# Optimization experiments

Hardware: AMD Instinct MI355X
Metric: run time of the kernel (lower is better)

Reference implementation:

```python
import jax, jax.numpy as jnp
import numpy as np

# ---- problem dims (match init_kwargs / input_specs) ----
B, N, ATOM = 128, 80, 16
HG, ENC_BLOCKS, ENC_HEADS, N_RBF = 512, 4, 8, 16
HID, DEC_LAYERS, DEC_HEADS = 256, 8, 8
KL_DIM, KL_WEIGHT = 6, 1e-6
NEG = -1e9


def layernorm(x, g, b, eps=1e-5):
    mu = x.mean(-1, keepdims=True)
    var = ((x - mu) ** 2).mean(-1, keepdims=True)
    return (x - mu) * jax.lax.rsqrt(var + eps) * g + b


def mha(x, qkv_w, qkv_b, out_w, out_b, bias, n_heads):
    # x: (B,S,D); bias: broadcastable to (B,H,S,S) additive attention bias/mask
    Bx, S, D = x.shape
    dh = D // n_heads
    q, k, v = jnp.split(x @ qkv_w + qkv_b, 3, axis=-1)
    q = q.reshape(Bx, S, n_heads, dh)
    k = k.reshape(Bx, S, n_heads, dh)
    v = v.reshape(Bx, S, n_heads, dh)
    logits = jnp.einsum('bqhd,bkhd->bhqk', q, k) * (1.0 / np.sqrt(dh)) + bias
    attn = jax.nn.softmax(logits, axis=-1)
    o = jnp.einsum('bhqk,bkhd->bqhd', attn, v).reshape(Bx, S, D)
    return o @ out_w + out_b


def sinusoid_posenc(seq_len, dim):
    pos = jnp.arange(seq_len, dtype=jnp.float32)[:, None]
    div = jnp.exp(jnp.arange(0, dim, 2, dtype=jnp.float32) * (-np.log(10000.0) / dim))
    ang = pos * div
    pe = jnp.zeros((seq_len, dim), jnp.float32)
    pe = pe.at[:, 0::2].set(jnp.sin(ang)).at[:, 1::2].set(jnp.cos(ang))
    return pe


def time_fourier(t, dim, max_len=200.0):
    half = dim // 2
    freqs = jnp.exp(jnp.arange(half, dtype=jnp.float32) * (-np.log(max_len) / half))
    ang = t[:, None] * max_len * freqs[None, :]
    return jnp.concatenate([jnp.sin(ang), jnp.cos(ang)], axis=-1)


def setup_inputs() -> dict:
    key = jax.random.key(0)
    ks = iter(jax.random.split(key, 64))
    nrm = lambda shp, s=0.02: jax.random.normal(next(ks), shp, jnp.float32) * s
    inp = {}
    inp['coord_ori'] = jax.random.normal(next(ks), (B, N, 3), jnp.float32)
    inp['atomics_ori'] = jax.nn.one_hot(jax.random.randint(next(ks), (B, N), 0, ATOM), ATOM, dtype=jnp.float32)
    lengths = jax.random.randint(next(ks), (B,), N // 2, N + 1)
    inp['padding_mask'] = jnp.arange(N)[None, :] >= lengths[:, None]
    inp['coord_t'] = jax.random.normal(next(ks), (B, N, 3), jnp.float32)
    inp['atomics_t'] = jax.nn.one_hot(jax.random.randint(next(ks), (B, N), 0, ATOM), ATOM, dtype=jnp.float32)
    inp['t'] = jax.random.uniform(next(ks), (B,), jnp.float32)
    # ---- GSRD encoder params (fully-connected graph attention blocks) ----
    inp['enc_embed_w'] = nrm((ATOM, HG))
    inp['rbf_w'] = nrm((ENC_BLOCKS, N_RBF, ENC_HEADS))
    inp['e_qkv_w'] = nrm((ENC_BLOCKS, HG, 3 * HG)); inp['e_qkv_b'] = jnp.zeros((ENC_BLOCKS, 3 * HG))
    inp['e_out_w'] = nrm((ENC_BLOCKS, HG, HG)); inp['e_out_b'] = jnp.zeros((ENC_BLOCKS, HG))
    inp['e_ff1_w'] = nrm((ENC_BLOCKS, HG, 4 * HG)); inp['e_ff1_b'] = jnp.zeros((ENC_BLOCKS, 4 * HG))
    inp['e_ff2_w'] = nrm((ENC_BLOCKS, 4 * HG, HG)); inp['e_ff2_b'] = jnp.zeros((ENC_BLOCKS, HG))
    inp['e_ln1_g'] = jnp.ones((ENC_BLOCKS, HG)); inp['e_ln1_b'] = jnp.zeros((ENC_BLOCKS, HG))
    inp['e_ln2_g'] = jnp.ones((ENC_BLOCKS, HG)); inp['e_ln2_b'] = jnp.zeros((ENC_BLOCKS, HG))
    # ---- projection / VAE bottleneck / decoder embeddings ----
    inp['enc_proj_w'] = nrm((HG, HID))
    inp['quant_w'] = nrm((HID, 2 * KL_DIM)); inp['quant_b'] = jnp.zeros((2 * KL_DIM,))
    inp['qout_w'] = nrm((KL_DIM, HID)); inp['qout_b'] = jnp.zeros((HID,))
    inp['cond_embed'] = nrm((2, HID))
    inp['lin_embed_w'] = nrm((3, HID))
    inp['atom_embed'] = nrm((ATOM, HID))
    # ---- decoder transformer (pre-norm, SiLU FFN) ----
    inp['d_qkv_w'] = nrm((DEC_LAYERS, HID, 3 * HID)); inp['d_qkv_b'] = jnp.zeros((DEC_LAYERS, 3 * HID))
    inp['d_out_w'] = nrm((DEC_LAYERS, HID, HID)); inp['d_out_b'] = jnp.zeros((DEC_LAYERS, HID))
    inp['d_ff1_w'] = nrm((DEC_LAYERS, HID, 4 * HID)); inp['d_ff1_b'] = jnp.zeros((DEC_LAYERS, 4 * HID))
    inp['d_ff2_w'] = nrm((DEC_LAYERS, 4 * HID, HID)); inp['d_ff2_b'] = jnp.zeros((DEC_LAYERS, HID))
    inp['d_ln1_g'] = jnp.ones((DEC_LAYERS, HID)); inp['d_ln1_b'] = jnp.zeros((DEC_LAYERS, HID))
    inp['d_ln2_g'] = jnp.ones((DEC_LAYERS, HID)); inp['d_ln2_b'] = jnp.zeros((DEC_LAYERS, HID))
    # ---- output heads ----
    inp['oc_ln_g'] = jnp.ones((HID,)); inp['oc_ln_b'] = jnp.zeros((HID,))
    inp['oc_w'] = nrm((HID, 3))
    inp['oa1_w'] = nrm((HID, HID)); inp['oa1_b'] = jnp.zeros((HID,))
    inp['oa2_w'] = nrm((HID, ATOM)); inp['oa2_b'] = jnp.zeros((ATOM,))
    return inp


def forward_impl(padding_mask, coord_ori, atomics_ori, coord_t, atomics_t, t,
                 enc_embed_w, rbf_w, e_qkv_w, e_qkv_b, e_out_w, e_out_b,
                 e_ff1_w, e_ff1_b, e_ff2_w, e_ff2_b, e_ln1_g, e_ln1_b, e_ln2_g, e_ln2_b,
                 enc_proj_w, quant_w, quant_b, qout_w, qout_b,
                 cond_embed, lin_embed_w, atom_embed,
                 d_qkv_w, d_qkv_b, d_out_w, d_out_b, d_ff1_w, d_ff1_b, d_ff2_w, d_ff2_b,
                 d_ln1_g, d_ln1_b, d_ln2_g, d_ln2_b,
                 oc_ln_g, oc_ln_b, oc_w, oa1_w, oa1_b, oa2_w, oa2_b):
    real = (~padding_mask).astype(jnp.float32)  # (B,N)
    # ===== encode_z: per-sample fully-connected graph GNN, expressed densely =====
    # The original builds (n*(n-1)) edges per molecule via meshgrid and runs an
    # edge-based encoder: equivalent to masked dense attention over (B,N,N) with
    # no self-loops and padded nodes removed.
    diff = coord_ori[:, :, None, :] - coord_ori[:, None, :, :]
    dist = jnp.sqrt((diff * diff).sum(-1) + 1e-12)                     # (B,N,N)
    centers = jnp.linspace(0.0, 10.0, N_RBF)
    rbf = jnp.exp(-2.0 * (dist[..., None] - centers) ** 2)             # (B,N,N,R)
    eye = jnp.eye(N, dtype=bool)
    emask = padding_mask[:, None, None, :] | eye[None, None, :, :]     # (B,1,N,N)
    mask_bias = jnp.where(emask, NEG, 0.0)
    h = atomics_ori @ enc_embed_w                                      # (B,N,HG)
    for i in range(ENC_BLOCKS):
        db = jnp.einsum('bqkr,rh->bhqk', rbf, rbf_w[i]) + mask_bias
        h = h + mha(layernorm(h, e_ln1_g[i], e_ln1_b[i]), e_qkv_w[i], e_qkv_b[i],
                    e_out_w[i], e_out_b[i], db, ENC_HEADS)
        f = layernorm(h, e_ln2_g[i], e_ln2_b[i])
        h = h + (jax.nn.silu(f @ e_ff1_w[i] + e_ff1_b[i]) @ e_ff2_w[i] + e_ff2_b[i])
    rep = h * real[..., None]                  # to_dense_batch zeros padded slots
    rep = rep @ enc_proj_w                     # (B,N,HID)
    # ---- VAE bottleneck (eval mode: z = mu) ----
    moments = rep @ quant_w + quant_b
    mu, logvar = jnp.split(moments, 2, axis=-1)
    z = mu
    kl_item = (1.0 + logvar - mu * mu - jnp.exp(logvar)) * real[..., None]
    kl_loss = -0.5 * jnp.mean(kl_item.sum(-1)) * KL_WEIGHT
    # ===== decode_z =====
    enc_emb = z @ qout_w + qout_b
    pe = sinusoid_posenc(N, HID)[None]         # (1,N,HID)
    enc_emb = (enc_emb + pe) * real[..., None]
    h_in = (coord_t @ lin_embed_w + atom_embed[atomics_t.argmax(-1)] + pe
            + time_fourier(t, HID)[:, None, :]) * real[..., None]
    x = jnp.concatenate([h_in, enc_emb], axis=1)                       # (B,2N,HID)
    x = x + jnp.concatenate([jnp.broadcast_to(cond_embed[0], (B, N, HID)),
                             jnp.broadcast_to(cond_embed[1], (B, N, HID))], axis=1)
    dmask = jnp.concatenate([padding_mask, padding_mask], axis=1)      # (B,2N)
    dbias = jnp.where(dmask, NEG, 0.0)[:, None, None, :]
    for i in range(DEC_LAYERS):
        x = x + mha(layernorm(x, d_ln1_g[i], d_ln1_b[i]), d_qkv_w[i], d_qkv_b[i],
                    d_out_w[i], d_out_b[i], dbias, DEC_HEADS)
        f = layernorm(x, d_ln2_g[i], d_ln2_b[i])
        x = x + (jax.nn.silu(f @ d_ff1_w[i] + d_ff1_b[i]) @ d_ff2_w[i] + d_ff2_b[i])
    h_out = x[:, :N, :] * real[..., None]
    coords = layernorm(h_out, oc_ln_g, oc_ln_b) @ oc_w
    atom_logits = jax.nn.silu(h_out @ oa1_w + oa1_b) @ oa2_w + oa2_b
    return coords, atom_logits, kl_loss


def reference(coord_ori, atomics_ori, padding_mask, coord_t, atomics_t, t,
              enc_embed_w, rbf_w, e_qkv_w, e_qkv_b, e_out_w, e_out_b,
              e_ff1_w, e_ff1_b, e_ff2_w, e_ff2_b, e_ln1_g, e_ln1_b, e_ln2_g, e_ln2_b,
              enc_proj_w, quant_w, quant_b, qout_w, qout_b,
              cond_embed, lin_embed_w, atom_embed,
              d_qkv_w, d_qkv_b, d_out_w, d_out_b, d_ff1_w, d_ff1_b, d_ff2_w, d_ff2_b,
              d_ln1_g, d_ln1_b, d_ln2_g, d_ln2_b,
              oc_ln_g, oc_ln_b, oc_w, oa1_w, oa1_b, oa2_w, oa2_b):
    return forward_impl(padding_mask, coord_ori, atomics_ori, coord_t, atomics_t, t,
                        enc_embed_w, rbf_w, e_qkv_w, e_qkv_b, e_out_w, e_out_b,
                        e_ff1_w, e_ff1_b, e_ff2_w, e_ff2_b, e_ln1_g, e_ln1_b, e_ln2_g, e_ln2_b,
                        enc_proj_w, quant_w, quant_b, qout_w, qout_b,
                        cond_embed, lin_embed_w, atom_embed,
                        d_qkv_w, d_qkv_b, d_out_w, d_out_b, d_ff1_w, d_ff1_b, d_ff2_w, d_ff2_b,
                        d_ln1_g, d_ln1_b, d_ln2_g, d_ln2_b,
                        oc_ln_g, oc_ln_b, oc_w, oa1_w, oa1_b, oa2_w, oa2_b)
```

## Files before the change

### kernel.cpp

```cpp
#include <hip/hip_runtime.h>
#include <hip/hip_bf16.h>
#include <math.h>

#define NBATCH 128
#define NATOM  80
#define SENC   80
#define SDEC   160
#define HGDIM  512
#define HIDDIM 256
#define NHEAD  8
#define ROWS_E (NBATCH*NATOM)
#define ROWS_D (NBATCH*SDEC)

typedef __hip_bfloat16 bf16;
typedef __attribute__((ext_vector_type(8))) short bf16x8;
typedef __attribute__((ext_vector_type(4))) float f32x4;

#define OFF_REAL 0ull
#define OFF_FLAG 10240ull
#define OFF_H    16384ull
#define OFF_QKVB (OFF_H   + 5242880ull)
#define OFF_DB   (OFF_QKVB+ 7864320ull)
#define OFF_LNB  (OFF_DB  + 6553600ull)
#define OFF_AOB  (OFF_LNB + 2621440ull)
#define OFF_MID  (OFF_AOB + 2621440ull)
#define OFF_MOM  (OFF_MID + 10485760ull)
#define OFF_KL   (OFF_MOM + 122880ull)
#define OFF_WT   (OFF_KL  + 64ull)
#define NEED_BYTES 184058112ull

#define WT_EQKV 0ull
#define WT_EOUT 3145728ull
#define WT_EFF1 4194304ull
#define WT_EFF2 8388608ull
#define WT_PROJ 12582912ull
#define WT_DQKV 12713984ull
#define WT_DOW  14286848ull
#define WT_DFF1 14811136ull
#define WT_DFF2 16908288ull
#define WT_OA1  19005440ull

static __device__ __forceinline__ float bu2f(unsigned int u){
  union{unsigned int i; float f;} x; x.i = u<<16; return x.f;
}
static __device__ __forceinline__ unsigned short f2bu(float f){
  union{bf16 h; unsigned short u;} x; x.h = __float2bfloat16(f); return x.u;
}

__global__ void k_maskmode(const unsigned char* __restrict__ m, int* __restrict__ flag){
  __shared__ int sh[256];
  int loc = 0;
  for(int i=threadIdx.x; i<ROWS_E; i+=256)
    if((i&3)!=0 && m[i]) loc = 1;
  sh[threadIdx.x] = loc;
  __syncthreads();
  if(threadIdx.x==0){
    int a=0;
    for(int j=0;j<256;j++) a |= sh[j];
    *flag = a;
  }
}

__global__ void k_real(const unsigned char* __restrict__ m, const int* __restrict__ flag,
                       float* __restrict__ real){
  int i = blockIdx.x*256 + threadIdx.x;
  if(i >= ROWS_E) return;
  int v = (*flag) ? (int)m[i] : ((const int*)m)[i];
  real[i] = v ? 0.f : 1.f;
}

__global__ void k_wsfail(float* __restrict__ out, float code){
  if(threadIdx.x==0) out[0] = code;
}

__global__ __launch_bounds__(256) void k_wt(const float* __restrict__ src,
    bf16* __restrict__ dst, int K, int N){
  __shared__ float t[32][33];
  const float* s = src + (size_t)blockIdx.z*K*N;
  bf16* d = dst + (size_t)blockIdx.z*K*N;
  int n0 = blockIdx.x*32, k0 = blockIdx.y*32;
  int tx = threadIdx.x & 31, ty = threadIdx.x >> 5;
  #pragma unroll
  for(int kk=0;kk<32;kk+=8)
    t[kk+ty][tx] = s[(size_t)(k0+kk+ty)*N + n0+tx];
  __syncthreads();
  #pragma unroll
  for(int nn=0;nn<32;nn+=8)
    d[(size_t)(n0+nn+ty)*K + k0+tx] = __float2bfloat16(t[tx][nn+ty]);
}

__global__ void k_embed(const float* __restrict__ atom, const float* __restrict__ W,
                        float* __restrict__ h){
  int idx = blockIdx.x*256 + threadIdx.x;
  if(idx >= ROWS_E*HGDIM) return;
  int row = idx >> 9, c = idx & 511;
  float s = 0.f;
  #pragma unroll
  for(int a=0;a<16;a++) s += atom[row*16+a] * W[a*HGDIM+c];
  h[idx] = s;
}

__global__ __launch_bounds__(256) void k_ln4(const float* __restrict__ x,
    const float* __restrict__ g, const float* __restrict__ bta,
    bf16* __restrict__ y, int D){
  int row = blockIdx.x*4 + (threadIdx.x>>6);
  int lane = threadIdx.x & 63;
  const float* xr = x + (size_t)row*D;
  int nch = D >> 8;
  float4 v[2];
  float s=0.f, s2=0.f;
  for(int j=0;j<nch;j++){
    v[j] = *(const float4*)&xr[j*256 + lane*4];
    s  += v[j].x+v[j].y+v[j].z+v[j].w;
    s2 += v[j].x*v[j].x+v[j].y*v[j].y+v[j].z*v[j].z+v[j].w*v[j].w;
  }
  #pragma unroll
  for(int o=32;o>0;o>>=1){ s += __shfl_xor(s,o); s2 += __shfl_xor(s2,o); }
  float mean = s / D;
  float var  = fmaxf(s2 / D - mean*mean, 0.f);
  float inv  = rsqrtf(var + 1e-5f);
  for(int j=0;j<nch;j++){
    int c = j*256 + lane*4;
    ushort4 o4;
    o4.x = f2bu((v[j].x-mean)*inv*g[c]   + bta[c]);
    o4.y = f2bu((v[j].y-mean)*inv*g[c+1] + bta[c+1]);
    o4.z = f2bu((v[j].z-mean)*inv*g[c+2] + bta[c+2]);
    o4.w = f2bu((v[j].w-mean)*inv*g[c+3] + bta[c+3]);
    *(ushort4*)&y[(size_t)row*D + c] = o4;
  }
}

__global__ __launch_bounds__(256) void k_ln4b(const bf16* __restrict__ x,
    const float* __restrict__ g, const float* __restrict__ bta,
    bf16* __restrict__ y, int D){
  int row = blockIdx.x*4 + (threadIdx.x>>6);
  int lane = threadIdx.x & 63;
  const unsigned short* xr = (const unsigned short*)(x + (size_t)row*D);
  int nch = D >> 8;
  float4 v[2];
  float s=0.f, s2=0.f;
  for(int j=0;j<nch;j++){
    ushort4 u = *(const ushort4*)&xr[j*256 + lane*4];
    v[j].x = bu2f(u.x); v[j].y = bu2f(u.y); v[j].z = bu2f(u.z); v[j].w = bu2f(u.w);
    s  += v[j].x+v[j].y+v[j].z+v[j].w;
    s2 += v[j].x*v[j].x+v[j].y*v[j].y+v[j].z*v[j].z+v[j].w*v[j].w;
  }
  #pragma unroll
  for(int o=32;o>0;o>>=1){ s += __shfl_xor(s,o); s2 += __shfl_xor(s2,o); }
  float mean = s / D;
  float var  = fmaxf(s2 / D - mean*mean, 0.f);
  float inv  = rsqrtf(var + 1e-5f);
  for(int j=0;j<nch;j++){
    int c = j*256 + lane*4;
    ushort4 o4;
    o4.x = f2bu((v[j].x-mean)*inv*g[c]   + bta[c]);
    o4.y = f2bu((v[j].y-mean)*inv*g[c+1] + bta[c+1]);
    o4.z = f2bu((v[j].z-mean)*inv*g[c+2] + bta[c+2]);
    o4.w = f2bu((v[j].w-mean)*inv*g[c+3] + bta[c+3]);
    *(ushort4*)&y[(size_t)row*D + c] = o4;
  }
}

__global__ void k_db(const float* __restrict__ coord, const float* __restrict__ real,
                     const float* __restrict__ rbfw, float* __restrict__ db){
  int idx = blockIdx.x*256 + threadIdx.x;
  if(idx >= NBATCH*SENC*SENC) return;
  int b = idx/(SENC*SENC), r = idx%(SENC*SENC), q = r/SENC, k = r%SENC;
  float out[NHEAD];
  bool masked = (real[b*NATOM+k]==0.f) || (k==q);
  if(masked){
    #pragma unroll
    for(int h=0;h<NHEAD;h++) out[h] = -1e9f;
  } else {
    float dx = coord[(b*NATOM+q)*3+0] - coord[(b*NATOM+k)*3+0];
    float dy = coord[(b*NATOM+q)*3+1] - coord[(b*NATOM+k)*3+1];
    float dz = coord[(b*NATOM+q)*3+2] - coord[(b*NATOM+k)*3+2];
    float d  = sqrtf(dx*dx+dy*dy+dz*dz + 1e-12f);
    #pragma unroll
    for(int h=0;h<NHEAD;h++) out[h]=0.f;
    for(int rr=0;rr<16;rr++){
      float cen = (10.f/15.f)*rr;
      float e = __expf(-2.f*(d-cen)*(d-cen));
      #pragma unroll
      for(int h=0;h<NHEAD;h++) out[h] += e * rbfw[rr*NHEAD+h];
    }
  }
  #pragma unroll
  for(int h=0;h<NHEAD;h++)
    db[(((size_t)b*NHEAD+h)*SENC + q)*SENC + k] = out[h];
}

#define MFMA_(acc, a, bfr) acc = __builtin_amdgcn_mfma_f32_16x16x32_bf16(a, bfr, acc, 0, 0, 0);

#define EQKT(kt, acc) { \
  bf16x8 bklo = *(const bf16x8*)&Ks[(kt)*16 + l15][g*8]; \
  bf16x8 bkhi = *(const bf16x8*)&Ks[(kt)*16 + l15][32 + g*8]; \
  MFMA_(acc, aqlo, bklo) MFMA_(acc, aqhi, bkhi) }
#define EBIAS(kt, sv) { \
  const float* dbr = dbb + (qt*16 + g*4)*80 + l15 + 16*(kt); \
  sv[0] = sv[0]*0.125f + dbr[0]; \
  sv[1] = sv[1]*0.125f + dbr[80]; \
  sv[2] = sv[2]*0.125f + dbr[160]; \
  sv[3] = sv[3]*0.125f + dbr[240]; }
#define EMAXJ(j) fmaxf(fmaxf(fmaxf(s0[j],s1[j]),fmaxf(s2[j],s3[j])),s4[j])
#define EEXP(sv) { sv[0]=__expf(sv[0]-m0); sv[1]=__expf(sv[1]-m1); sv[2]=__expf(sv[2]-m2); sv[3]=__expf(sv[3]-m3); }
#define ESUMJ(j) (s0[j]+s1[j]+s2[j]+s3[j]+s4[j])
#define ESTP(kt, sv) { \
  Pw[w][g*4+0][l15+16*(kt)] = f2bu(sv[0]); \
  Pw[w][g*4+1][l15+16*(kt)] = f2bu(sv[1]); \
  Pw[w][g*4+2][l15+16*(kt)] = f2bu(sv[2]); \
  Pw[w][g*4+3][l15+16*(kt)] = f2bu(sv[3]); }
#define EST(ov, ct) { \
  ob[0*HGDIM + (ct)*16 + l15] = __float2bfloat16(ov[0]*i0); \
  ob[1*HGDIM + (ct)*16 + l15] = __float2bfloat16(ov[1]*i1); \
  ob[2*HGDIM + (ct)*16 + l15] = __float2bfloat16(ov[2]*i2); \
  ob[3*HGDIM + (ct)*16 + l15] = __float2bfloat16(ov[3]*i3); }

__global__ __launch_bounds__(256) void k_attn_enc3(
    const bf16* __restrict__ qkvb, const float* __restrict__ db,
    bf16* __restrict__ o_out)
{
  __shared__ unsigned short Qs[80][72];
  __shared__ unsigned short Ks[80][72];
  __shared__ unsigned short Vt[64][104];
  __shared__ unsigned short Pw[4][16][104];
  int bh = blockIdx.x; int h = bh & 7, b = bh >> 3;
  const bf16* base = qkvb + (size_t)b*SENC*1536;
  const float* dbb = db + (size_t)bh*6400;
  int tid = threadIdx.x;
  int w = tid >> 6, lane = tid & 63;
  int l15 = lane & 15, g = lane >> 4;
  for(int c = tid; c < 640; c += 256){
    int r = c >> 3, p = c & 7;
    *(uint4*)&Qs[r][p*8] = *(const uint4*)(base + (size_t)r*1536 + h*64 + p*8);
    *(uint4*)&Ks[r][p*8] = *(const uint4*)(base + (size_t)r*1536 + 512 + h*64 + p*8);
  }
  for(int c = tid; c < 80*64; c += 256){
    int k = c >> 6, d = c & 63;
    Vt[d][k] = *(const unsigned short*)(base + (size_t)k*1536 + 1024 + h*64 + d);
  }
  for(int c = tid; c < 64*16; c += 256){
    int d = c >> 4, cc = c & 15;
    Vt[d][80+cc] = 0;
  }
  {
    int r = lane >> 2, c4 = (lane & 3)*4;
    ushort4 zz = {0,0,0,0};
    *(ushort4*)&Pw[w][r][80 + c4] = zz;
  }
  __syncthreads();
  for(int qt = w; qt < 5; qt += 4){
    bf16x8 aqlo = *(const bf16x8*)&Qs[qt*16 + l15][g*8];
    bf16x8 aqhi = *(const bf16x8*)&Qs[qt*16 + l15][32 + g*8];
    f32x4 z = {0.f,0.f,0.f,0.f};
    f32x4 s0=z,s1=z,s2=z,s3=z,s4=z;
    EQKT(0,s0) EQKT(1,s1) EQKT(2,s2) EQKT(3,s3) EQKT(4,s4)
    EBIAS(0,s0) EBIAS(1,s1) EBIAS(2,s2) EBIAS(3,s3) EBIAS(4,s4)
    float m0=EMAXJ(0), m1=EMAXJ(1), m2=EMAXJ(2), m3=EMAXJ(3);
    #pragma unroll
    for(int off=1; off<16; off<<=1){
      m0 = fmaxf(m0, __shfl_xor(m0, off));
      m1 = fmaxf(m1, __shfl_xor(m1, off));
      m2 = fmaxf(m2, __shfl_xor(m2, off));
      m3 = fmaxf(m3, __shfl_xor(m3, off));
    }
    EEXP(s0) EEXP(s1) EEXP(s2) EEXP(s3) EEXP(s4)
    float l0=ESUMJ(0), l1=ESUMJ(1), l2=ESUMJ(2), l3=ESUMJ(3);
    #pragma unroll
    for(int off=1; off<16; off<<=1){
      l0 += __shfl_xor(l0, off);
      l1 += __shfl_xor(l1, off);
      l2 += __shfl_xor(l2, off);
      l3 += __shfl_xor(l3, off);
    }
    ESTP(0,s0) ESTP(1,s1) ESTP(2,s2) ESTP(3,s3) ESTP(4,s4)
    f32x4 o0=z, o1=z, o2=z, o3=z;
    #pragma unroll
    for(int kc=0; kc<3; kc++){
      bf16x8 ap = *(const bf16x8*)&Pw[w][l15][kc*32 + g*8];
      bf16x8 v0 = *(const bf16x8*)&Vt[l15][kc*32 + g*8];
      bf16x8 v1 = *(const bf16x8*)&Vt[16 + l15][kc*32 + g*8];
      bf16x8 v2 = *(const bf16x8*)&Vt[32 + l15][kc*32 + g*8];
      bf16x8 v3 = *(const bf16x8*)&Vt[48 + l15][kc*32 + g*8];
      MFMA_(o0, ap, v0) MFMA_(o1, ap, v1) MFMA_(o2, ap, v2) MFMA_(o3, ap, v3)
    }
    float i0 = 1.f/l0, i1 = 1.f/l1, i2 = 1.f/l2, i3 = 1.f/l3;
    bf16* ob = o_out + ((size_t)(b*SENC + qt*16 + g*4))*HGDIM + h*64;
    EST(o0, 0) EST(o1, 1) EST(o2, 2) EST(o3, 3)
  }
}

#define QKT(kt, acc) { bf16x8 bk = *(const bf16x8*)&Ks[(kt)*16 + l15][g*8]; MFMA_(acc, aq, bk) }
#define SMSC(sv, mbv) { sv[0]=sv[0]*SCAL+(mbv); sv[1]=sv[1]*SCAL+(mbv); sv[2]=sv[2]*SCAL+(mbv); sv[3]=sv[3]*SCAL+(mbv); }
#define MAXJ(j) fmaxf(fmaxf(fmaxf(fmaxf(s0[j],s1[j]),fmaxf(s2[j],s3[j])),fmaxf(fmaxf(s4[j],s5[j]),fmaxf(s6[j],s7[j]))),fmaxf(s8[j],s9[j]))
#define EXPS(sv) { sv[0]=__expf(sv[0]-m0); sv[1]=__expf(sv[1]-m1); sv[2]=__expf(sv[2]-m2); sv[3]=__expf(sv[3]-m3); }
#define SUMJ(j) (s0[j]+s1[j]+s2[j]+s3[j]+s4[j]+s5[j]+s6[j]+s7[j]+s8[j]+s9[j])
#define STP(kt, sv) { \
  Pw[w][g*4+0][l15+16*(kt)] = f2bu(sv[0]); \
  Pw[w][g*4+1][l15+16*(kt)] = f2bu(sv[1]); \
  Pw[w][g*4+2][l15+16*(kt)] = f2bu(sv[2]); \
  Pw[w][g*4+3][l15+16*(kt)] = f2bu(sv[3]); }

__global__ __launch_bounds__(256) void k_attn_dec5(
    const bf16* __restrict__ qkvb, const float* __restrict__ real,
    bf16* __restrict__ o_out)
{
  __shared__ unsigned short Qs[160][40];
  __shared__ unsigned short Ks[160][40];
  __shared__ unsigned short Vt[32][168];
  __shared__ unsigned short Pw[4][16][168];
  __shared__ float mb[160];
  const float SCAL = 0.17677669529663689f;
  int bh = blockIdx.x; int h = bh & 7, b = bh >> 3;
  const bf16* base = qkvb + (size_t)b*SDEC*768;
  int tid = threadIdx.x;
  int w = tid >> 6, lane = tid & 63;
  int l15 = lane & 15, g = lane >> 4;
  for(int c = tid; c < 160*4; c += 256){
    int r = c >> 2, p = c & 3;
    *(uint4*)&Qs[r][p*8] = *(const uint4*)(base + (size_t)r*768 + h*32 + p*8);
    *(uint4*)&Ks[r][p*8] = *(const uint4*)(base + (size_t)r*768 + 256 + h*32 + p*8);
  }
  for(int c = tid; c < 160*32; c += 256){
    int k = c >> 5, d = c & 31;
    Vt[d][k] = *(const unsigned short*)(base + (size_t)k*768 + 512 + h*32 + d);
  }
  for(int k = tid; k < 160; k += 256){
    int kk = (k<80)?k:k-80;
    mb[k] = (real[b*NATOM+kk]==0.f) ? -1e9f : 0.f;
  }
  __syncthreads();
  float mb0=mb[l15],     mb1=mb[l15+16],  mb2=mb[l15+32],  mb3=mb[l15+48],  mb4=mb[l15+64];
  float mb5=mb[l15+80],  mb6=mb[l15+96],  mb7=mb[l15+112], mb8=mb[l15+128], mb9=mb[l15+144];
  for(int qt = w; qt < 10; qt += 4){
    bf16x8 aq = *(const bf16x8*)&Qs[qt*16 + l15][g*8];
    f32x4 z = {0.f,0.f,0.f,0.f};
    f32x4 s0=z,s1=z,s2=z,s3=z,s4=z,s5=z,s6=z,s7=z,s8=z,s9=z;
    QKT(0,s0) QKT(1,s1) QKT(2,s2) QKT(3,s3) QKT(4,s4)
    QKT(5,s5) QKT(6,s6) QKT(7,s7) QKT(8,s8) QKT(9,s9)
    SMSC(s0,mb0) SMSC(s1,mb1) SMSC(s2,mb2) SMSC(s3,mb3) SMSC(s4,mb4)
    SMSC(s5,mb5) SMSC(s6,mb6) SMSC(s7,mb7) SMSC(s8,mb8) SMSC(s9,mb9)
    float m0=MAXJ(0), m1=MAXJ(1), m2=MAXJ(2), m3=MAXJ(3);
    #pragma unroll
    for(int off=1; off<16; off<<=1){
      m0 = fmaxf(m0, __shfl_xor(m0, off));
      m1 = fmaxf(m1, __shfl_xor(m1, off));
      m2 = fmaxf(m2, __shfl_xor(m2, off));
      m3 = fmaxf(m3, __shfl_xor(m3, off));
    }
    EXPS(s0) EXPS(s1) EXPS(s2) EXPS(s3) EXPS(s4)
    EXPS(s5) EXPS(s6) EXPS(s7) EXPS(s8) EXPS(s9)
    float l0=SUMJ(0), l1=SUMJ(1), l2=SUMJ(2), l3=SUMJ(3);
    #pragma unroll
    for(int off=1; off<16; off<<=1){
      l0 += __shfl_xor(l0, off);
      l1 += __shfl_xor(l1, off);
      l2 += __shfl_xor(l2, off);
      l3 += __shfl_xor(l3, off);
    }
    STP(0,s0) STP(1,s1) STP(2,s2) STP(3,s3) STP(4,s4)
    STP(5,s5) STP(6,s6) STP(7,s7) STP(8,s8) STP(9,s9)
    f32x4 o0 = z, o1 = z;
    #pragma unroll
    for(int kt=0; kt<5; kt++){
      bf16x8 ap = *(const bf16x8*)&Pw[w][l15][kt*32 + g*8];
      bf16x8 v0 = *(const bf16x8*)&Vt[l15][kt*32 + g*8];
      bf16x8 v1 = *(const bf16x8*)&Vt[16 + l15][kt*32 + g*8];
      MFMA_(o0, ap, v0)
      MFMA_(o1, ap, v1)
    }
    float i0 = 1.f/l0, i1 = 1.f/l1, i2 = 1.f/l2, i3 = 1.f/l3;
    bf16* ob = o_out + ((size_t)(b*SDEC + qt*16 + g*4))*HIDDIM + h*32;
    ob[0*HIDDIM + l15]      = __float2bfloat16(o0[0]*i0);
    ob[1*HIDDIM + l15]      = __float2bfloat16(o0[1]*i1);
    ob[2*HIDDIM + l15]      = __float2bfloat16(o0[2]*i2);
    ob[3*HIDDIM + l15]      = __float2bfloat16(o0[3]*i3);
    ob[0*HIDDIM + 16 + l15] = __float2bfloat16(o1[0]*i0);
    ob[1*HIDDIM + 16 + l15] = __float2bfloat16(o1[1]*i1);
    ob[2*HIDDIM + 16 + l15] = __float2bfloat16(o1[2]*i2);
    ob[3*HIDDIM + 16 + l15] = __float2bfloat16(o1[3]*i3);
  }
}

#define MFM(accv, av, bv) accv = __builtin_amdgcn_mfma_f32_16x16x32_bf16(av, bv, accv, 0, 0, 0);
#define EPIM(accv, rr, cc) { \
  int col = col0 + (cc)*16 + l15; \
  float bi = bias ? bias[col] : 0.f; \
  _Pragma("unroll") \
  for(int j=0;j<4;j++){ \
    int row = row0 + w*32 + (rr)*16 + g*4 + j; \
    float v = accv[j] + bi; \
    if(resid) v += resid[(size_t)row*Nw + col]; \
    if(act==1) v = v/(1.f+__expf(-v)); \
    if(Cf) Cf[(size_t)row*Nw + col] = v; \
    else   Cb[(size_t)row*Nw + col] = __float2bfloat16(v); } }

#define SUBSTEP(s) { \
  int ch = ((s)*4 + g) ^ sw7; \
  bf16x8 a0 = *(const bf16x8*)&As4[w*32 + l15][ch]; \
  bf16x8 a1 = *(const bf16x8*)&As4[w*32 + 16 + l15][ch]; \
  bf16x8 b0 = *(const bf16x8*)&Bs4[l15][ch]; \
  bf16x8 b1 = *(const bf16x8*)&Bs4[16 + l15][ch]; \
  bf16x8 b2 = *(const bf16x8*)&Bs4[32 + l15][ch]; \
  bf16x8 b3 = *(const bf16x8*)&Bs4[48 + l15][ch]; \
  bf16x8 b4 = *(const bf16x8*)&Bs4[64 + l15][ch]; \
  bf16x8 b5 = *(const bf16x8*)&Bs4[80 + l15][ch]; \
  bf16x8 b6 = *(const bf16x8*)&Bs4[96 + l15][ch]; \
  bf16x8 b7 = *(const bf16x8*)&Bs4[112 + l15][ch]; \
  MFM(c00, a0, b0) MFM(c01, a0, b1) MFM(c02, a0, b2) MFM(c03, a0, b3) \
  MFM(c04, a0, b4) MFM(c05, a0, b5) MFM(c06, a0, b6) MFM(c07, a0, b7) \
  MFM(c10, a1, b0) MFM(c11, a1, b1) MFM(c12, a1, b2) MFM(c13, a1, b3) \
  MFM(c14, a1, b4) MFM(c15, a1, b5) MFM(c16, a1, b6) MFM(c17, a1, b7) }

__global__ __launch_bounds__(256) void k_gemm_mfma5(
    const bf16* __restrict__ A, const bf16* __restrict__ WT,
    const float* __restrict__ bias, const float* __restrict__ resid,
    float* __restrict__ Cf, bf16* __restrict__ Cb,
    int M, int K, int Nw, int act)
{
  __shared__ uint4 As4[128][8];
  __shared__ uint4 Bs4[128][8];
  int tid = threadIdx.x;
  int w = tid >> 6, lane = tid & 63;
  int l15 = lane & 15, g = lane >> 4;
  int row0 = blockIdx.y*128, col0 = blockIdx.x*128;
  int arow = tid >> 1, ahalf = tid & 1;
  int swr = arow & 7;
  int sw7 = l15 & 7;
  int bb = ahalf*4;
  f32x4 z = {0.f,0.f,0.f,0.f};
  f32x4 c00=z,c01=z,c02=z,c03=z,c04=z,c05=z,c06=z,c07=z;
  f32x4 c10=z,c11=z,c12=z,c13=z,c14=z,c15=z,c16=z,c17=z;
  for(int k0=0;k0<K;k0+=64){
    const uint4* asrc = (const uint4*)(A  + (size_t)(row0+arow)*K + k0 + ahalf*32);
    const uint4* bsrc = (const uint4*)(WT + (size_t)(col0+arow)*K + k0 + ahalf*32);
    uint4 av0 = asrc[0], av1 = asrc[1], av2 = asrc[2], av3 = asrc[3];
    uint4 bv0 = bsrc[0], bv1 = bsrc[1], bv2 = bsrc[2], bv3 = bsrc[3];
    As4[arow][(bb+0)^swr] = av0;
    As4[arow][(bb+1)^swr] = av1;
    As4[arow][(bb+2)^swr] = av2;
    As4[arow][(bb+3)^swr] = av3;
    Bs4[arow][(bb+0)^swr] = bv0;
    Bs4[arow][(bb+1)^swr] = bv1;
    Bs4[arow][(bb+2)^swr] = bv2;
    Bs4[arow][(bb+3)^swr] = bv3;
    __syncthreads();
    SUBSTEP(0)
    SUBSTEP(1)
    __syncthreads();
  }
  EPIM(c00, 0, 0) EPIM(c01, 0, 1) EPIM(c02, 0, 2) EPIM(c03, 0, 3)
  EPIM(c04, 0, 4) EPIM(c05, 0, 5) EPIM(c06, 0, 6) EPIM(c07, 0, 7)
  EPIM(c10, 1, 0) EPIM(c11, 1, 1) EPIM(c12, 1, 2) EPIM(c13, 1, 3)
  EPIM(c14, 1, 4) EPIM(c15, 1, 5) EPIM(c16, 1, 6) EPIM(c17, 1, 7)
}

#define EPIM6(accv, rr, cc) { \
  int col = col0 + w*32 + (cc)*16 + l15; \
  float bi = bias ? bias[col] : 0.f; \
  _Pragma("unroll") \
  for(int j=0;j<4;j++){ \
    int row = row0 + (rr)*16 + g*4 + j; \
    float v = accv[j] + bi; \
    if(resid) v += resid[(size_t)row*Nw + col]; \
    if(act==1) v = v/(1.f+__expf(-v)); \
    if(Cf) Cf[(size_t)row*Nw + col] = v; \
    else   Cb[(size_t)row*Nw + col] = __float2bfloat16(v); } }

#define SUBSTEP6(s) { \
  int ch = ((s)*4 + g) ^ sw7; \
  bf16x8 a0 = *(const bf16x8*)&As4[l15][ch]; \
  bf16x8 a1 = *(const bf16x8*)&As4[16 + l15][ch]; \
  bf16x8 a2 = *(const bf16x8*)&As4[32 + l15][ch]; \
  bf16x8 a3 = *(const bf16x8*)&As4[48 + l15][ch]; \
  bf16x8 b0 = *(const bf16x8*)&Bs4[w*32 + l15][ch]; \
  bf16x8 b1 = *(const bf16x8*)&Bs4[w*32 + 16 + l15][ch]; \
  MFM(c00, a0, b0) MFM(c01, a0, b1) \
  MFM(c10, a1, b0) MFM(c11, a1, b1) \
  MFM(c20, a2, b0) MFM(c21, a2, b1) \
  MFM(c30, a3, b0) MFM(c31, a3, b1) }

__global__ __launch_bounds__(256) void k_gemm_mfma6(
    const bf16* __restrict__ A, const bf16* __restrict__ WT,
    const float* __restrict__ bias, const float* __restrict__ resid,
    float* __restrict__ Cf, bf16* __restrict__ Cb,
    int M, int K, int Nw, int act)
{
  __shared__ uint4 As4[64][8];
  __shared__ uint4 Bs4[128][8];
  int tid = threadIdx.x;
  int w = tid >> 6, lane = tid & 63;
  int l15 = lane & 15, g = lane >> 4;
  int row0 = blockIdx.y*64, col0 = blockIdx.x*128;
  int arow4 = tid >> 2, aq = tid & 3;
  int swA = arow4 & 7;
  int brow = tid >> 1, bhalf = tid & 1;
  int swB = brow & 7;
  int sw7 = l15 & 7;
  f32x4 z = {0.f,0.f,0.f,0.f};
  f32x4 c00=z,c01=z,c10=z,c11=z,c20=z,c21=z,c30=z,c31=z;
  for(int k0=0;k0<K;k0+=64){
    const uint4* asrc = (const uint4*)(A  + (size_t)(row0+arow4)*K + k0 + aq*16);
    const uint4* bsrc = (const uint4*)(WT + (size_t)(col0+brow)*K + k0 + bhalf*32);
    uint4 av0 = asrc[0], av1 = asrc[1];
    uint4 bv0 = bsrc[0], bv1 = bsrc[1], bv2 = bsrc[2], bv3 = bsrc[3];
    As4[arow4][(2*aq+0)^swA] = av0;
    As4[arow4][(2*aq+1)^swA] = av1;
    int bb = bhalf*4;
    Bs4[brow][(bb+0)^swB] = bv0;
    Bs4[brow][(bb+1)^swB] = bv1;
    Bs4[brow][(bb+2)^swB] = bv2;
    Bs4[brow][(bb+3)^swB] = bv3;
    __syncthreads();
    SUBSTEP6(0)
    SUBSTEP6(1)
    __syncthreads();
  }
  EPIM6(c00, 0, 0) EPIM6(c01, 0, 1)
  EPIM6(c10, 1, 0) EPIM6(c11, 1, 1)
  EPIM6(c20, 2, 0) EPIM6(c21, 2, 1)
  EPIM6(c30, 3, 0) EPIM6(c31, 3, 1)
}

__global__ void k_gemm_small(const bf16* __restrict__ A, const float* __restrict__ W,
    const float* __restrict__ bias, float* __restrict__ C,
    int M, int K, int Nw, int act){
  int idx = blockIdx.x*256 + threadIdx.x;
  if(idx >= M*Nw) return;
  int row = idx / Nw, col = idx % Nw;
  float s = bias ? bias[col] : 0.f;
  const bf16* a = A + (size_t)row*K;
  for(int k=0;k<K;k++) s += __bfloat162float(a[k])*W[(size_t)k*Nw+col];
  if(act==1) s = s/(1.f+__expf(-s));
  C[idx] = s;
}

__global__ __launch_bounds__(256) void k_kl(const float* __restrict__ mom,
    const float* __restrict__ real, float* __restrict__ part){
  int i = blockIdx.x*256 + threadIdx.x;
  float s = 0.f;
  if(i < ROWS_E){
    const float* m = mom + (size_t)i*12;
    float acc = 0.f;
    #pragma unroll
    for(int d=0;d<6;d++){ float mu=m[d], lv=m[6+d]; acc += 1.f + lv - mu*mu - expf(lv); }
    s = acc * real[i];
  }
  #pragma unroll
  for(int o=32;o>0;o>>=1) s += __shfl_xor(s,o);
  __shared__ float r[4];
  if((threadIdx.x&63)==0) r[threadIdx.x>>6]=s;
  __syncthreads();
  if(threadIdx.x==0) part[blockIdx.x] = r[0]+r[1]+r[2]+r[3];
}

__global__ void k_klfin(const float* __restrict__ part, float* __restrict__ o){
  float s=0.f;
  for(int i=0;i<40;i++) s += part[i];
  *o = -0.5f * (s/(float)ROWS_E) * 1e-6f;
}

__global__ void k_cvtrs(const float* __restrict__ h, const float* __restrict__ real,
                        bf16* __restrict__ o){
  int idx = blockIdx.x*256 + threadIdx.x;
  if(idx >= ROWS_E*HGDIM) return;
  int row = idx >> 9;
  o[idx] = __float2bfloat16(h[idx]*real[row]);
}

__global__ __launch_bounds__(256) void k_build_x(
  const float* __restrict__ coord_t, const float* __restrict__ atomics_t, const float* __restrict__ tin,
  const float* __restrict__ qout_w, const float* __restrict__ qout_b, const float* __restrict__ cond,
  const float* __restrict__ lin_w, const float* __restrict__ atom_emb,
  const float* __restrict__ mom, const float* __restrict__ real, float* __restrict__ x)
{
  int idx = blockIdx.x*256 + threadIdx.x;
  if(idx >= NBATCH*SDEC*HIDDIM) return;
  int c = idx & 255; int rowg = idx >> 8; int s = rowg % SDEC; int b = rowg / SDEC;
  int n = (s<NATOM)? s : s-NATOM;
  int j = c >> 1;
  float div = __expf(-(float)(2*j) * (9.210340371976184f/256.f));
  float ang = (float)n * div;
  float pe = (c & 1) ? __cosf(ang) : __sinf(ang);
  float rl = real[b*NATOM + n];
  float v;
  if(s < NATOM){
    int rown = b*NATOM + n;
    float cl = 0.f;
    #pragma unroll
    for(int a=0;a<3;a++) cl += coord_t[rown*3+a] * lin_w[a*HIDDIM+c];
    int bi=0; float bv = atomics_t[rown*16];
    for(int a=1;a<16;a++){ float vv=atomics_t[rown*16+a]; if(vv>bv){bv=vv; bi=a;} }
    float ae = atom_emb[bi*HIDDIM+c];
    float tb = tin[b];
    float tf;
    if(c < 128){
      float fr = __expf(-(float)c * (5.298317366548036f/128.f));
      tf = __sinf(tb*200.f*fr);
    } else {
      float fr = __expf(-(float)(c-128) * (5.298317366548036f/128.f));
      tf = __cosf(tb*200.f*fr);
    }
    v = (cl + ae + pe + tf)*rl + cond[c];
  } else {
    int rown = b*NATOM + n;
    const float* mp = mom + (size_t)rown*12;
    float s2 = qout_b[c];
    #pragma unroll
    for(int d=0;d<6;d++) s2 += mp[d]*qout_w[d*HIDDIM+c];
    v = (s2 + pe)*rl + cond[HIDDIM+c];
  }
  x[idx] = v;
}

__global__ void k_hout(const float* __restrict__ x, const float* __restrict__ real,
                       bf16* __restrict__ h_out_b){
  int idx = blockIdx.x*256 + threadIdx.x;
  if(idx >= ROWS_E*HIDDIM) return;
  int c = idx & 255, row = idx >> 8;
  int n = row % NATOM, b = row / NATOM;
  float v = x[((size_t)(b*SDEC+n))*HIDDIM + c] * real[row];
  h_out_b[idx] = __float2bfloat16(v);
}

extern "C" void kernel_launch(void* const* d_in, const int* in_sizes, int n_in,
                              void* d_out, int out_size, void* d_ws, size_t ws_size,
                              hipStream_t stream){
  (void)in_sizes; (void)n_in; (void)out_size;
  const float* coord_ori   = (const float*)d_in[0];
  const float* atomics_ori = (const float*)d_in[1];
  const unsigned char* pmask = (const unsigned char*)d_in[2];
  const float* coord_t     = (const float*)d_in[3];
  const float* atomics_t   = (const float*)d_in[4];
  const float* t_in        = (const float*)d_in[5];
  const float* enc_embed_w = (const float*)d_in[6];
  const float* rbf_w       = (const float*)d_in[7];
  const float* e_qkv_w=(const float*)d_in[8];  const float* e_qkv_b=(const float*)d_in[9];
  const float* e_out_w=(const float*)d_in[10]; const float* e_out_b=(const float*)d_in[11];
  const float* e_ff1_w=(const float*)d_in[12]; const float* e_ff1_b=(const float*)d_in[13];
  const float* e_ff2_w=(const float*)d_in[14]; const float* e_ff2_b=(const float*)d_in[15];
  const float* e_ln1_g=(const float*)d_in[16]; const float* e_ln1_b=(const float*)d_in[17];
  const float* e_ln2_g=(const float*)d_in[18]; const float* e_ln2_b=(const float*)d_in[19];
  const float* enc_proj_w=(const float*)d_in[20];
  const float* quant_w=(const float*)d_in[21]; const float* quant_b=(const float*)d_in[22];
  const float* qout_w=(const float*)d_in[23];  const float* qout_b=(const float*)d_in[24];
  const float* cond_embed=(const float*)d_in[25];
  const float* lin_embed_w=(const float*)d_in[26];
  const float* atom_embed=(const float*)d_in[27];
  const float* d_qkv_w=(const float*)d_in[28]; const float* d_qkv_b=(const float*)d_in[29];
  const float* d_ow   =(const float*)d_in[30]; const float* d_ob   =(const float*)d_in[31];
  const float* d_ff1_w=(const float*)d_in[32]; const float* d_ff1_b=(const float*)d_in[33];
  const float* d_ff2_w=(const float*)d_in[34]; const float* d_ff2_b=(const float*)d_in[35];
  const float* d_ln1_g=(const float*)d_in[36]; const float* d_ln1_b=(const float*)d_in[37];
  const float* d_ln2_g=(const float*)d_in[38]; const float* d_ln2_b=(const float*)d_in[39];
  const float* oc_ln_g=(const float*)d_in[40]; const float* oc_ln_b=(const float*)d_in[41];
  const float* oc_w   =(const float*)d_in[42];
  const float* oa1_w  =(const float*)d_in[43]; const float* oa1_b=(const float*)d_in[44];
  const float* oa2_w  =(const float*)d_in[45]; const float* oa2_b=(const float*)d_in[46];

  float* ws   = (float*)d_ws;
  float* real = ws + OFF_REAL;
  int*   flag = (int*)(ws + OFF_FLAG);
  float* h    = ws + OFF_H;
  bf16*  qkvb = (bf16*)(ws + OFF_QKVB);
  float* db   = ws + OFF_DB;
  bf16*  lnb  = (bf16*)(ws + OFF_LNB);
  bf16*  aob  = (bf16*)(ws + OFF_AOB);
  bf16*  mid  = (bf16*)(ws + OFF_MID);
  float* mom  = ws + OFF_MOM;
  float* klp  = ws + OFF_KL;
  bf16*  wt   = (bf16*)(ws + OFF_WT);
  float* out  = (float*)d_out;

  if(ws_size < NEED_BYTES){
    k_wsfail<<<1,64,0,stream>>>(out, 1.0e6f + (float)(ws_size>>20));
    return;
  }

  k_wt<<<dim3(48,16,4),256,0,stream>>>(e_qkv_w,  wt+WT_EQKV, 512, 1536);
  k_wt<<<dim3(16,16,4),256,0,stream>>>(e_out_w,  wt+WT_EOUT, 512, 512);
  k_wt<<<dim3(64,16,4),256,0,stream>>>(e_ff1_w,  wt+WT_EFF1, 512, 2048);
  k_wt<<<dim3(16,64,4),256,0,stream>>>(e_ff2_w,  wt+WT_EFF2, 2048, 512);
  k_wt<<<dim3(8,16,1), 256,0,stream>>>(enc_proj_w, wt+WT_PROJ, 512, 256);
  k_wt<<<dim3(24,8,8), 256,0,stream>>>(d_qkv_w,  wt+WT_DQKV, 256, 768);
  k_wt<<<dim3(8,8,8),  256,0,stream>>>(d_ow,     wt+WT_DOW,  256, 256);
  k_wt<<<dim3(32,8,8), 256,0,stream>>>(d_ff1_w,  wt+WT_DFF1, 256, 1024);
  k_wt<<<dim3(8,32,8), 256,0,stream>>>(d_ff2_w,  wt+WT_DFF2, 1024, 256);
  k_wt<<<dim3(8,8,1),  256,0,stream>>>(oa1_w,    wt+WT_OA1,  256, 256);

  k_maskmode<<<1,256,0,stream>>>(pmask, flag);
  k_real <<<40,   256, 0, stream>>>(pmask, flag, real);
  k_embed<<<20480,256, 0, stream>>>(atomics_ori, enc_embed_w, h);

  for(int i=0;i<4;i++){
    k_ln4<<<ROWS_E/4,256,0,stream>>>(h, e_ln1_g+i*HGDIM, e_ln1_b+i*HGDIM, lnb, HGDIM);
    k_gemm_mfma5<<<dim3(12,80),256,0,stream>>>(lnb, wt+WT_EQKV+(size_t)i*512*1536,
        e_qkv_b+i*3*HGDIM, nullptr, nullptr, qkvb, ROWS_E, HGDIM, 3*HGDIM, 0);
    k_db<<<3200,256,0,stream>>>(coord_ori, real, rbf_w + i*16*NHEAD, db);
    k_attn_enc3<<<NBATCH*NHEAD,256,0,stream>>>(qkvb, db, aob);
    k_gemm_mfma6<<<dim3(4,160),256,0,stream>>>(aob, wt+WT_EOUT+(size_t)i*512*512,
        e_out_b+i*HGDIM, h, h, nullptr, ROWS_E, HGDIM, HGDIM, 0);
    k_ln4<<<ROWS_E/4,256,0,stream>>>(h, e_ln2_g+i*HGDIM, e_ln2_b+i*HGDIM, lnb, HGDIM);
    k_gemm_mfma5<<<dim3(16,80),256,0,stream>>>(lnb, wt+WT_EFF1+(size_t)i*512*2048,
        e_ff1_b+i*4*HGDIM, nullptr, nullptr, mid, ROWS_E, HGDIM, 4*HGDIM, 1);
    k_gemm_mfma6<<<dim3(4,160),256,0,stream>>>(mid, wt+WT_EFF2+(size_t)i*2048*512,
        e_ff2_b+i*HGDIM, h, h, nullptr, ROWS_E, 4*HGDIM, HGDIM, 0);
  }

  k_cvtrs<<<20480,256,0,stream>>>(h, real, lnb);
  k_gemm_mfma6<<<dim3(2,160),256,0,stream>>>(lnb, wt+WT_PROJ,
      nullptr, nullptr, nullptr, aob, ROWS_E, HGDIM, HIDDIM, 0);
  k_gemm_small<<<480,256,0,stream>>>(aob, quant_w, quant_b, mom, ROWS_E, HIDDIM, 12, 0);
  k_kl   <<<40,256,0,stream>>>(mom, real, klp);
  k_klfin<<<1,1,0,stream>>>(klp, out + 194560);

  k_build_x<<<20480,256,0,stream>>>(coord_t, atomics_t, t_in, qout_w, qout_b,
      cond_embed, lin_embed_w, atom_embed, mom, real, h);

  for(int i=0;i<8;i++){
    k_ln4<<<ROWS_D/4,256,0,stream>>>(h, d_ln1_g+i*HIDDIM, d_ln1_b+i*HIDDIM, lnb, HIDDIM);
    k_gemm_mfma6<<<dim3(6,320),256,0,stream>>>(lnb, wt+WT_DQKV+(size_t)i*256*768,
        d_qkv_b+i*3*HIDDIM, nullptr, nullptr, qkvb, ROWS_D, HIDDIM, 3*HIDDIM, 0);
    k_attn_dec5<<<NBATCH*NHEAD,256,0,stream>>>(qkvb, real, aob);
    k_gemm_mfma6<<<dim3(2,320),256,0,stream>>>(aob, wt+WT_DOW+(size_t)i*256*256,
        d_ob+i*HIDDIM, h, h, nullptr, ROWS_D, HIDDIM, HIDDIM, 0);
    k_ln4<<<ROWS_D/4,256,0,stream>>>(h, d_ln2_g+i*HIDDIM, d_ln2_b+i*HIDDIM, lnb, HIDDIM);
    k_gemm_mfma5<<<dim3(8,160),256,0,stream>>>(lnb, wt+WT_DFF1+(size_t)i*256*1024,
        d_ff1_b+i*4*HIDDIM, nullptr, nullptr, mid, ROWS_D, HIDDIM, 4*HIDDIM, 1);
    k_gemm_mfma6<<<dim3(2,320),256,0,stream>>>(mid, wt+WT_DFF2+(size_t)i*1024*256,
        d_ff2_b+i*HIDDIM, h, h, nullptr, ROWS_D, 4*HIDDIM, HIDDIM, 0);
  }

  k_hout<<<10240,256,0,stream>>>(h, real, aob);
  k_ln4b<<<ROWS_E/4,256,0,stream>>>(aob, oc_ln_g, oc_ln_b, lnb, HIDDIM);
  k_gemm_small<<<120,256,0,stream>>>(lnb, oc_w, nullptr, out, ROWS_E, HIDDIM, 3, 0);
  k_gemm_mfma6<<<dim3(2,160),256,0,stream>>>(aob, wt+WT_OA1, oa1_b, nullptr,
      nullptr, mid, ROWS_E, HIDDIM, HIDDIM, 1);
  k_gemm_small<<<640,256,0,stream>>>(mid, oa2_w, oa2_b, out + 30720,
      ROWS_E, HIDDIM, 16, 0);
}
```

Baseline: 2.927 ms.

## Prefetch next K-tile into registers and reorder GEMM block mapping column-major

```diff
diff --git a/kernel.cpp b/kernel.cpp
--- a/kernel.cpp
+++ b/kernel.cpp
@@ -412,7 +412,7 @@
   MFM(c10, a1, b0) MFM(c11, a1, b1) MFM(c12, a1, b2) MFM(c13, a1, b3) \
   MFM(c14, a1, b4) MFM(c15, a1, b5) MFM(c16, a1, b6) MFM(c17, a1, b7) }
 
-__global__ __launch_bounds__(256) void k_gemm_mfma5(
+__global__ __launch_bounds__(256) void k_gemm_mfma7(
     const bf16* __restrict__ A, const bf16* __restrict__ WT,
     const float* __restrict__ bias, const float* __restrict__ resid,
     float* __restrict__ Cf, bf16* __restrict__ Cb,
@@ -423,19 +423,27 @@
   int tid = threadIdx.x;
   int w = tid >> 6, lane = tid & 63;
   int l15 = lane & 15, g = lane >> 4;
-  int row0 = blockIdx.y*128, col0 = blockIdx.x*128;
+  int lin = blockIdx.x + gridDim.x*blockIdx.y;
+  int bcol = lin / gridDim.y;
+  int brw  = lin - bcol*gridDim.y;
+  int row0 = brw*128, col0 = bcol*128;
   int arow = tid >> 1, ahalf = tid & 1;
   int swr = arow & 7;
   int sw7 = l15 & 7;
   int bb = ahalf*4;
+  const bf16* aP = A  + (size_t)(row0+arow)*K + ahalf*32;
+  const bf16* bP = WT + (size_t)(col0+arow)*K + ahalf*32;
   f32x4 z = {0.f,0.f,0.f,0.f};
   f32x4 c00=z,c01=z,c02=z,c03=z,c04=z,c05=z,c06=z,c07=z;
   f32x4 c10=z,c11=z,c12=z,c13=z,c14=z,c15=z,c16=z,c17=z;
+  uint4 av0,av1,av2,av3,bv0,bv1,bv2,bv3;
+  {
+    const uint4* asrc = (const uint4*)aP;
+    const uint4* bsrc = (const uint4*)bP;
+    av0=asrc[0]; av1=asrc[1]; av2=asrc[2]; av3=asrc[3];
+    bv0=bsrc[0]; bv1=bsrc[1]; bv2=bsrc[2]; bv3=bsrc[3];
+  }
   for(int k0=0;k0<K;k0+=64){
-    const uint4* asrc = (const uint4*)(A  + (size_t)(row0+arow)*K + k0 + ahalf*32);
-    const uint4* bsrc = (const uint4*)(WT + (size_t)(col0+arow)*K + k0 + ahalf*32);
-    uint4 av0 = asrc[0], av1 = asrc[1], av2 = asrc[2], av3 = asrc[3];
-    uint4 bv0 = bsrc[0], bv1 = bsrc[1], bv2 = bsrc[2], bv3 = bsrc[3];
     As4[arow][(bb+0)^swr] = av0;
     As4[arow][(bb+1)^swr] = av1;
     As4[arow][(bb+2)^swr] = av2;
@@ -445,6 +453,13 @@
     Bs4[arow][(bb+2)^swr] = bv2;
     Bs4[arow][(bb+3)^swr] = bv3;
     __syncthreads();
+    int kn = k0 + 64;
+    if(kn < K){
+      const uint4* asrc = (const uint4*)(aP + kn);
+      const uint4* bsrc = (const uint4*)(bP + kn);
+      av0=asrc[0]; av1=asrc[1]; av2=asrc[2]; av3=asrc[3];
+      bv0=bsrc[0]; bv1=bsrc[1]; bv2=bsrc[2]; bv3=bsrc[3];
+    }
     SUBSTEP(0)
     SUBSTEP(1)
     __syncthreads();
@@ -455,7 +470,7 @@
   EPIM(c14, 1, 4) EPIM(c15, 1, 5) EPIM(c16, 1, 6) EPIM(c17, 1, 7)
 }
 
-#define EPIM6(accv, rr, cc) { \
+#define EPIM8(accv, rr, cc) { \
   int col = col0 + w*32 + (cc)*16 + l15; \
   float bi = bias ? bias[col] : 0.f; \
   _Pragma("unroll") \
@@ -467,7 +482,7 @@
     if(Cf) Cf[(size_t)row*Nw + col] = v; \
     else   Cb[(size_t)row*Nw + col] = __float2bfloat16(v); } }
 
-#define SUBSTEP6(s) { \
+#define SUBSTEP8(s) { \
   int ch = ((s)*4 + g) ^ sw7; \
   bf16x8 a0 = *(const bf16x8*)&As4[l15][ch]; \
   bf16x8 a1 = *(const bf16x8*)&As4[16 + l15][ch]; \
@@ -480,7 +495,7 @@
   MFM(c20, a2, b0) MFM(c21, a2, b1) \
   MFM(c30, a3, b0) MFM(c31, a3, b1) }
 
-__global__ __launch_bounds__(256) void k_gemm_mfma6(
+__global__ __launch_bounds__(256) void k_gemm_mfma8(
     const bf16* __restrict__ A, const bf16* __restrict__ WT,
     const float* __restrict__ bias, const float* __restrict__ resid,
     float* __restrict__ Cf, bf16* __restrict__ Cb,
@@ -491,19 +506,27 @@
   int tid = threadIdx.x;
   int w = tid >> 6, lane = tid & 63;
   int l15 = lane & 15, g = lane >> 4;
-  int row0 = blockIdx.y*64, col0 = blockIdx.x*128;
+  int lin = blockIdx.x + gridDim.x*blockIdx.y;
+  int bcol = lin / gridDim.y;
+  int brw  = lin - bcol*gridDim.y;
+  int row0 = brw*64, col0 = bcol*128;
   int arow4 = tid >> 2, aq = tid & 3;
   int swA = arow4 & 7;
   int brow = tid >> 1, bhalf = tid & 1;
   int swB = brow & 7;
   int sw7 = l15 & 7;
+  const bf16* aP = A  + (size_t)(row0+arow4)*K + aq*16;
+  const bf16* bP = WT + (size_t)(col0+brow)*K + bhalf*32;
   f32x4 z = {0.f,0.f,0.f,0.f};
   f32x4 c00=z,c01=z,c10=z,c11=z,c20=z,c21=z,c30=z,c31=z;
+  uint4 av0,av1,bv0,bv1,bv2,bv3;
+  {
+    const uint4* asrc = (const uint4*)aP;
+    const uint4* bsrc = (const uint4*)bP;
+    av0=asrc[0]; av1=asrc[1];
+    bv0=bsrc[0]; bv1=bsrc[1]; bv2=bsrc[2]; bv3=bsrc[3];
+  }
   for(int k0=0;k0<K;k0+=64){
-    const uint4* asrc = (const uint4*)(A  + (size_t)(row0+arow4)*K + k0 + aq*16);
-    const uint4* bsrc = (const uint4*)(WT + (size_t)(col0+brow)*K + k0 + bhalf*32);
-    uint4 av0 = asrc[0], av1 = asrc[1];
-    uint4 bv0 = bsrc[0], bv1 = bsrc[1], bv2 = bsrc[2], bv3 = bsrc[3];
     As4[arow4][(2*aq+0)^swA] = av0;
     As4[arow4][(2*aq+1)^swA] = av1;
     int bb = bhalf*4;
@@ -512,14 +535,21 @@
     Bs4[brow][(bb+2)^swB] = bv2;
     Bs4[brow][(bb+3)^swB] = bv3;
     __syncthreads();
-    SUBSTEP6(0)
-    SUBSTEP6(1)
+    int kn = k0 + 64;
+    if(kn < K){
+      const uint4* asrc = (const uint4*)(aP + kn);
+      const uint4* bsrc = (const uint4*)(bP + kn);
+      av0=asrc[0]; av1=asrc[1];
+      bv0=bsrc[0]; bv1=bsrc[1]; bv2=bsrc[2]; bv3=bsrc[3];
+    }
+    SUBSTEP8(0)
+    SUBSTEP8(1)
     __syncthreads();
   }
-  EPIM6(c00, 0, 0) EPIM6(c01, 0, 1)
-  EPIM6(c10, 1, 0) EPIM6(c11, 1, 1)
-  EPIM6(c20, 2, 0) EPIM6(c21, 2, 1)
-  EPIM6(c30, 3, 0) EPIM6(c31, 3, 1)
+  EPIM8(c00, 0, 0) EPIM8(c01, 0, 1)
+  EPIM8(c10, 1, 0) EPIM8(c11, 1, 1)
+  EPIM8(c20, 2, 0) EPIM8(c21, 2, 1)
+  EPIM8(c30, 3, 0) EPIM8(c31, 3, 1)
 }
 
 __global__ void k_gemm_small(const bf16* __restrict__ A, const float* __restrict__ W,
@@ -694,21 +724,21 @@
 
   for(int i=0;i<4;i++){
     k_ln4<<<ROWS_E/4,256,0,stream>>>(h, e_ln1_g+i*HGDIM, e_ln1_b+i*HGDIM, lnb, HGDIM);
-    k_gemm_mfma5<<<dim3(12,80),256,0,stream>>>(lnb, wt+WT_EQKV+(size_t)i*512*1536,
+    k_gemm_mfma7<<<dim3(12,80),256,0,stream>>>(lnb, wt+WT_EQKV+(size_t)i*512*1536,
         e_qkv_b+i*3*HGDIM, nullptr, nullptr, qkvb, ROWS_E, HGDIM, 3*HGDIM, 0);
     k_db<<<3200,256,0,stream>>>(coord_ori, real, rbf_w + i*16*NHEAD, db);
     k_attn_enc3<<<NBATCH*NHEAD,256,0,stream>>>(qkvb, db, aob);
-    k_gemm_mfma6<<<dim3(4,160),256,0,stream>>>(aob, wt+WT_EOUT+(size_t)i*512*512,
+    k_gemm_mfma8<<<dim3(4,160),256,0,stream>>>(aob, wt+WT_EOUT+(size_t)i*512*512,
         e_out_b+i*HGDIM, h, h, nullptr, ROWS_E, HGDIM, HGDIM, 0);
     k_ln4<<<ROWS_E/4,256,0,stream>>>(h, e_ln2_g+i*HGDIM, e_ln2_b+i*HGDIM, lnb, HGDIM);
-    k_gemm_mfma5<<<dim3(16,80),256,0,stream>>>(lnb, wt+WT_EFF1+(size_t)i*512*2048,
+    k_gemm_mfma7<<<dim3(16,80),256,0,stream>>>(lnb, wt+WT_EFF1+(size_t)i*512*2048,
         e_ff1_b+i*4*HGDIM, nullptr, nullptr, mid, ROWS_E, HGDIM, 4*HGDIM, 1);
-    k_gemm_mfma6<<<dim3(4,160),256,0,stream>>>(mid, wt+WT_EFF2+(size_t)i*2048*512,
+    k_gemm_mfma8<<<dim3(4,160),256,0,stream>>>(mid, wt+WT_EFF2+(size_t)i*2048*512,
         e_ff2_b+i*HGDIM, h, h, nullptr, ROWS_E, 4*HGDIM, HGDIM, 0);
   }
 
   k_cvtrs<<<20480,256,0,stream>>>(h, real, lnb);
-  k_gemm_mfma6<<<dim3(2,160),256,0,stream>>>(lnb, wt+WT_PROJ,
+  k_gemm_mfma8<<<dim3(2,160),256,0,stream>>>(lnb, wt+WT_PROJ,
       nullptr, nullptr, nullptr, aob, ROWS_E, HGDIM, HIDDIM, 0);
   k_gemm_small<<<480,256,0,stream>>>(aob, quant_w, quant_b, mom, ROWS_E, HIDDIM, 12, 0);
   k_kl   <<<40,256,0,stream>>>(mom, real, klp);
@@ -719,22 +749,22 @@
 
   for(int i=0;i<8;i++){
     k_ln4<<<ROWS_D/4,256,0,stream>>>(h, d_ln1_g+i*HIDDIM, d_ln1_b+i*HIDDIM, lnb, HIDDIM);
-    k_gemm_mfma6<<<dim3(6,320),256,0,stream>>>(lnb, wt+WT_DQKV+(size_t)i*256*768,
+    k_gemm_mfma8<<<dim3(6,320),256,0,stream>>>(lnb, wt+WT_DQKV+(size_t)i*256*768,
         d_qkv_b+i*3*HIDDIM, nullptr, nullptr, qkvb, ROWS_D, HIDDIM, 3*HIDDIM, 0);
     k_attn_dec5<<<NBATCH*NHEAD,256,0,stream>>>(qkvb, real, aob);
-    k_gemm_mfma6<<<dim3(2,320),256,0,stream>>>(aob, wt+WT_DOW+(size_t)i*256*256,
+    k_gemm_mfma8<<<dim3(2,320),256,0,stream>>>(aob, wt+WT_DOW+(size_t)i*256*256,
         d_ob+i*HIDDIM, h, h, nullptr, ROWS_D, HIDDIM, HIDDIM, 0);
     k_ln4<<<ROWS_D/4,256,0,stream>>>(h, d_ln2_g+i*HIDDIM, d_ln2_b+i*HIDDIM, lnb, HIDDIM);
-    k_gemm_mfma5<<<dim3(8,160),256,0,stream>>>(lnb, wt+WT_DFF1+(size_t)i*256*1024,
+    k_gemm_mfma7<<<dim3(8,160),256,0,stream>>>(lnb, wt+WT_DFF1+(size_t)i*256*1024,
         d_ff1_b+i*4*HIDDIM, nullptr, nullptr, mid, ROWS_D, HIDDIM, 4*HIDDIM, 1);
-    k_gemm_mfma6<<<dim3(2,320),256,0,stream>>>(mid, wt+WT_DFF2+(size_t)i*1024*256,
+    k_gemm_mfma8<<<dim3(2,320),256,0,stream>>>(mid, wt+WT_DFF2+(size_t)i*1024*256,
         d_ff2_b+i*HIDDIM, h, h, nullptr, ROWS_D, 4*HIDDIM, HIDDIM, 0);
   }
 
   k_hout<<<10240,256,0,stream>>>(h, real, aob);
   k_ln4b<<<ROWS_E/4,256,0,stream>>>(aob, oc_ln_g, oc_ln_b, lnb, HIDDIM);
   k_gemm_small<<<120,256,0,stream>>>(lnb, oc_w, nullptr, out, ROWS_E, HIDDIM, 3, 0);
-  k_gemm_mfma6<<<dim3(2,160),256,0,stream>>>(aob, wt+WT_OA1, oa1_b, nullptr,
+  k_gemm_mfma8<<<dim3(2,160),256,0,stream>>>(aob, wt+WT_OA1, oa1_b, nullptr,
       nullptr, mid, ROWS_E, HIDDIM, HIDDIM, 1);
   k_gemm_small<<<640,256,0,stream>>>(mid, oa2_w, oa2_b, out + 30720,
       ROWS_E, HIDDIM, 16, 0);
```

Result: faster. 2.791 ms (-4.6%).
